# Kernel tuning notes

Measured on AMD Instinct MI355X. Metric: run time of the kernel, lower is better.

The kernel has to match this reference:

```python
import jax, jax.numpy as jnp
import numpy as np

K, B, N, F, D_CONST = 2, 100000, 1000, 500, 14

def setup_inputs() -> dict:
    key = jax.random.key(0)
    ks = jax.random.split(key, 7)
    height = jax.random.uniform(ks[0], (K, B), dtype=jnp.float32) * 3000.0 + 100.0
    width = jax.random.uniform(ks[1], (K, B), dtype=jnp.float32) * 1.0 + 1.0  # spot width in pixels
    x = jax.random.normal(ks[2], (K, B), dtype=jnp.float32)  # sub-pixel offset from target
    y = jax.random.normal(ks[3], (K, B), dtype=jnp.float32)
    target_locs = jax.random.uniform(ks[4], (N, F, 2), dtype=jnp.float32) * (D_CONST - 1)
    n_idx = jax.random.randint(ks[5], (B,), 0, N)
    f_idx = jax.random.randint(ks[6], (B,), 0, F)
    return {"height": height, "width": width, "x": x, "y": y,
            "target_locs": target_locs, "n_idx": n_idx, "f_idx": f_idx, "D": D_CONST}

def reference(height, width, x, y, target_locs, n_idx, f_idx, D):
    # pixel grid [D, D, 2], 'ij' indexing like torch.meshgrid default
    r = jnp.arange(D, dtype=jnp.float32)
    ii, jj = jnp.meshgrid(r, r, indexing="ij")
    ij_pixel = jnp.stack((ii, jj), axis=-1)  # [D, D, 2]
    # gather target locations and add sub-pixel offsets -> [K, B, 2]
    spot_locs = target_locs[n_idx, f_idx] + jnp.stack((x, y), axis=-1)
    # isotropic 2D Gaussian: MVN with scale_tril = eye(2)*width
    diff = ij_pixel - spot_locs[:, :, None, None, :]  # [K, B, D, D, 2]
    w2 = (width * width)[:, :, None, None]  # [K, B, 1, 1]
    log_prob = -0.5 * jnp.sum(diff * diff, axis=-1) / w2 \
               - jnp.log(2.0 * jnp.pi) - jnp.log(w2)
    gaussian_spot = jnp.exp(log_prob)  # [K, B, D, D]
    return height[:, :, None, None] * gaussian_spot
```

## Files before the change

### kernel.cpp

```cpp
#include <hip/hip_runtime.h>


#define KB_TOTAL 200000u
#define B_NUM    100000u
#define F_NUM    500
#define D_DIM    14u
#define F4_PER_SPOT 49u
#define TOTAL_F4 (KB_TOTAL * F4_PER_SPOT)

__global__ __launch_bounds__(256) void gspot_kernel(
    const float* __restrict__ height,
    const float* __restrict__ width,
    const float* __restrict__ xoff,
    const float* __restrict__ yoff,
    const float* __restrict__ tlocs,
    const int*   __restrict__ n_idx,
    const int*   __restrict__ f_idx,
    float4*      __restrict__ out)
{
    const float HALF_LOG2E = 0.7213475204444817f;
    const float INV_2PI    = 0.15915494309189535f;

    unsigned stride = gridDim.x * blockDim.x;
    for (unsigned t = blockIdx.x * blockDim.x + threadIdx.x; t < TOTAL_F4; t += stride) {
        unsigned spot = t / F4_PER_SPOT;
        unsigned q    = t - spot * F4_PER_SPOT;
        unsigned b    = spot % B_NUM;

        float h  = height[spot];
        float w  = width[spot];
        float sx = xoff[spot];
        float sy = yoff[spot];

        int n = n_idx[b];
        int f = f_idx[b];
        const float* tl = tlocs + ((unsigned)(n * F_NUM + f)) * 2u;
        sx += tl[0];
        sy += tl[1];

        float w2    = w * w;
        float inv   = __builtin_amdgcn_rcpf(w2);
        float scale = h * inv * INV_2PI;
        float c     = -HALF_LOG2E * inv;

        unsigned p0 = q * 4u;
        float e[4];
        #pragma unroll
        for (int m = 0; m < 4; ++m) {
            unsigned p = p0 + (unsigned)m;
            unsigned i = p / D_DIM;
            unsigned j = p - i * D_DIM;
            float di = (float)i - sx;
            float dj = (float)j - sy;
            float s  = di * di + dj * dj;
            e[m] = scale * __builtin_amdgcn_exp2f(s * c);
        }
        out[t] = make_float4(e[0], e[1], e[2], e[3]);
    }
}

extern "C" void kernel_launch(void* const* d_in, const int* in_sizes, int n_in,
                              void* d_out, int out_size, void* d_ws, size_t ws_size,
                              hipStream_t stream) {
    const float* height = (const float*)d_in[0];
    const float* width  = (const float*)d_in[1];
    const float* x      = (const float*)d_in[2];
    const float* y      = (const float*)d_in[3];
    const float* tlocs  = (const float*)d_in[4];
    const int*   n_idx  = (const int*)d_in[5];
    const int*   f_idx  = (const int*)d_in[6];
    float4* out = (float4*)d_out;

    dim3 grid(2048), block(256);
    hipLaunchKernelGGL(gspot_kernel, grid, block, 0, stream,
                       height, width, x, y, tlocs, n_idx, f_idx, out);
}
```

Measured before the change: 39.09 us.

## Factor Gaussian into separable row/column exponentials staged in shared memory

```diff
diff --git a/kernel.cpp b/kernel.cpp
--- a/kernel.cpp
+++ b/kernel.cpp
@@ -1,12 +1,12 @@
 #include <hip/hip_runtime.h>
 
 
-#define KB_TOTAL 200000u
-#define B_NUM    100000u
-#define F_NUM    500
-#define D_DIM    14u
-#define F4_PER_SPOT 49u
-#define TOTAL_F4 (KB_TOTAL * F4_PER_SPOT)
+#define S_SPOTS 100
+#define NBLK    (200000 / S_SPOTS)
+#define B_NUM   100000u
+#define F_NUM   500
+#define D_DIM   14u
+#define LSTRIDE 16u
 
 __global__ __launch_bounds__(256) void gspot_kernel(
     const float* __restrict__ height,
@@ -18,44 +18,67 @@
     const int*   __restrict__ f_idx,
     float4*      __restrict__ out)
 {
+    __shared__ float sp_sx[S_SPOTS], sp_sy[S_SPOTS], sp_c[S_SPOTS], sp_sc[S_SPOTS];
+    __shared__ float ex[S_SPOTS * LSTRIDE];
+    __shared__ float ey[S_SPOTS * LSTRIDE];
+
     const float HALF_LOG2E = 0.7213475204444817f;
     const float INV_2PI    = 0.15915494309189535f;
 
-    unsigned stride = gridDim.x * blockDim.x;
-    for (unsigned t = blockIdx.x * blockDim.x + threadIdx.x; t < TOTAL_F4; t += stride) {
-        unsigned spot = t / F4_PER_SPOT;
-        unsigned q    = t - spot * F4_PER_SPOT;
+    const unsigned tid = threadIdx.x;
+    const unsigned spot_base = blockIdx.x * S_SPOTS;
+
+    if (tid < S_SPOTS) {
+        unsigned spot = spot_base + tid;
         unsigned b    = spot % B_NUM;
-
         float h  = height[spot];
         float w  = width[spot];
         float sx = xoff[spot];
         float sy = yoff[spot];
-
         int n = n_idx[b];
         int f = f_idx[b];
         const float* tl = tlocs + ((unsigned)(n * F_NUM + f)) * 2u;
         sx += tl[0];
         sy += tl[1];
+        float inv = __builtin_amdgcn_rcpf(w * w);
+        sp_sx[tid] = sx;
+        sp_sy[tid] = sy;
+        sp_c[tid]  = -HALF_LOG2E * inv;
+        sp_sc[tid] = h * inv * INV_2PI;
+    }
+    __syncthreads();
 
-        float w2    = w * w;
-        float inv   = __builtin_amdgcn_rcpf(w2);
-        float scale = h * inv * INV_2PI;
-        float c     = -HALF_LOG2E * inv;
+    for (unsigned item = tid; item < S_SPOTS * 2u * D_DIM; item += 256u) {
+        unsigned sp = item / (2u * D_DIM);
+        unsigned r  = item - sp * (2u * D_DIM);
+        float c = sp_c[sp];
+        if (r < D_DIM) {
+            float d = (float)r - sp_sx[sp];
+            ex[sp * LSTRIDE + r] = sp_sc[sp] * __builtin_amdgcn_exp2f(c * d * d);
+        } else {
+            unsigned j = r - D_DIM;
+            float d = (float)j - sp_sy[sp];
+            ey[sp * LSTRIDE + j] = __builtin_amdgcn_exp2f(c * d * d);
+        }
+    }
+    __syncthreads();
 
+    float4* outb = out + (size_t)spot_base * 49u;
+    for (unsigned idx = tid; idx < S_SPOTS * 49u; idx += 256u) {
+        unsigned sp = idx / 49u;
+        unsigned q  = idx - sp * 49u;
         unsigned p0 = q * 4u;
+        const float* exb = ex + sp * LSTRIDE;
+        const float* eyb = ey + sp * LSTRIDE;
         float e[4];
         #pragma unroll
         for (int m = 0; m < 4; ++m) {
             unsigned p = p0 + (unsigned)m;
             unsigned i = p / D_DIM;
             unsigned j = p - i * D_DIM;
-            float di = (float)i - sx;
-            float dj = (float)j - sy;
-            float s  = di * di + dj * dj;
-            e[m] = scale * __builtin_amdgcn_exp2f(s * c);
+            e[m] = exb[i] * eyb[j];
         }
-        out[t] = make_float4(e[0], e[1], e[2], e[3]);
+        outb[idx] = make_float4(e[0], e[1], e[2], e[3]);
     }
 }
 
@@ -71,7 +94,6 @@
     const int*   f_idx  = (const int*)d_in[6];
     float4* out = (float4*)d_out;
 
-    dim3 grid(2048), block(256);
-    hipLaunchKernelGGL(gspot_kernel, grid, block, 0, stream,
+    hipLaunchKernelGGL(gspot_kernel, dim3(NBLK), dim3(256), 0, stream,
                        height, width, x, y, tlocs, n_idx, f_idx, out);
 }
```

Result: faster. 33.12 us (-15.3%).
